# Optimization experiments

Measured on AMD Instinct MI355X. Metric: run time of the kernel, lower is better.

The kernel has to match this reference:

```python
import jax, jax.numpy as jnp
import numpy as np

B, L, C, K, NLEV, VOCAB, OUT = 32, 1024, 512, 2, 4, 128, 11


def setup_inputs() -> dict:
    key = jax.random.key(0)
    ks = jax.random.split(key, 8)
    x = jax.random.randint(ks[0], (B, L), 0, VOCAB, dtype=jnp.int32)
    mask = jax.random.randint(ks[1], (B, L), 0, 2).astype(jnp.bool_)
    emb = jax.random.uniform(ks[2], (VOCAB, C), minval=-0.5, maxval=0.5, dtype=jnp.float32)
    w1 = jax.random.normal(ks[3], (NLEV, C, C, K), dtype=jnp.float32) * 0.02
    b1 = jnp.zeros((NLEV, C), dtype=jnp.float32)
    w2 = jax.random.normal(ks[4], (NLEV, C, C, K), dtype=jnp.float32) * 0.02
    b2 = jnp.zeros((NLEV, C), dtype=jnp.float32)
    dec_w = jax.random.uniform(ks[5], (OUT, C), minval=-0.5, maxval=0.5, dtype=jnp.float32)
    dec_b = jnp.zeros((OUT,), dtype=jnp.float32)
    return dict(x=x, mask=mask, emb=emb, w1=w1, b1=b1, w2=w2, b2=b2, dec_w=dec_w, dec_b=dec_b)


def _causal_conv(h, w, b, dilation):
    # h: [B, C, L], w: [Cout, Cin, K]; left-pad (K-1)*d == conv+chomp in TCN
    pad = (w.shape[-1] - 1) * dilation
    out = jax.lax.conv_general_dilated(
        h, w, window_strides=(1,), padding=[(pad, 0)],
        rhs_dilation=(dilation,), dimension_numbers=("NCH", "OIH", "NCH"))
    return out + b[None, :, None]


def reference(x, mask, emb, w1, b1, w2, b2, dec_w, dec_b):
    h = emb[x].transpose(0, 2, 1)  # [B, C, L]
    for i in range(NLEV):  # fixed small number of TCN levels
        d = 2 ** i
        res = h
        h = jax.nn.relu(_causal_conv(h, w1[i], b1[i], d))
        h = jax.nn.relu(_causal_conv(h, w2[i], b2[i], d))
        h = jax.nn.relu(h + res)  # residual (in==out channels -> identity shortcut)
    y = jnp.einsum("bcl,oc->blo", h, dec_w) + dec_b  # [B, L, OUT]
    # mask-gather: original keeps only mask-true positions; zero others (jit-safe)
    return y * mask[..., None].astype(y.dtype)
```

## Files before the change

kernel.cpp:

```cpp
#include <hip/hip_runtime.h>
#include <stdint.h>

#define BB 32
#define LL 1024
#define CC 512
#define NN (BB * LL)
#define NLEVS 4
#define OUTD 11
#define LPAD 8
#define LROWS (LL + LPAD)

typedef __attribute__((ext_vector_type(8))) short bf16x8;
typedef __attribute__((ext_vector_type(4))) float f32x4;

static __device__ __forceinline__ unsigned short f2bf(float f) {
    union { float f; uint32_t u; } v; v.f = f;
    uint32_t u = v.u;
    uint32_t r = (u + 0x7fffu + ((u >> 16) & 1u)) >> 16;
    return (unsigned short)r;
}
static __device__ __forceinline__ float bf2f(unsigned short h) {
    union { uint32_t u; float f; } v; v.u = ((uint32_t)h) << 16;
    return v.f;
}

static __device__ __forceinline__ void llds16(const unsigned short* g, unsigned short* l) {
    __builtin_amdgcn_global_load_lds(
        (const __attribute__((address_space(1))) unsigned int*)g,
        (__attribute__((address_space(3))) unsigned int*)l, 16, 0, 0);
}

__global__ __launch_bounds__(256) void zero_pad_kernel(
    unsigned short* __restrict__ Hb0, unsigned short* __restrict__ Hb1)
{
    int t = blockIdx.x * 256 + threadIdx.x;
    unsigned short* base = (t >> 14) ? Hb1 : Hb0;
    int rem = t & 16383;
    int p = rem >> 9;
    int q = rem & 511;
    size_t off = (size_t)p * (LROWS * CC) + (size_t)q * 8;
    *(uint4*)(base + off) = (uint4){0u, 0u, 0u, 0u};
}

__global__ __launch_bounds__(256) void embed_kernel(
    const int* __restrict__ x, const float* __restrict__ emb,
    unsigned short* __restrict__ Hb0)
{
    int t = blockIdx.x * 256 + threadIdx.x;
    int n = t >> 6;
    int c8 = (t & 63) * 8;
    int idx = x[n];
    const float* src = emb + (size_t)idx * CC + c8;
    float4 v0 = *(const float4*)src;
    float4 v1 = *(const float4*)(src + 4);
    ushort4 a, b;
    a.x = f2bf(v0.x); a.y = f2bf(v0.y); a.z = f2bf(v0.z); a.w = f2bf(v0.w);
    b.x = f2bf(v1.x); b.y = f2bf(v1.y); b.z = f2bf(v1.z); b.w = f2bf(v1.w);
    int prow = (n >> 10) * LROWS + LPAD + (n & (LL - 1));
    unsigned short* dst = Hb0 + (size_t)prow * CC + c8;
    *(ushort4*)dst = a;
    *(ushort4*)(dst + 4) = b;
}

__global__ __launch_bounds__(256) void pack_w_kernel(
    const float* __restrict__ w1, const float* __restrict__ w2, unsigned short* __restrict__ WpT)
{
    int e = blockIdx.x * 256 + threadIdx.x;
    int cv = e >> 19;
    int r = e & 524287;
    int j = r >> 12;
    int co = (r >> 3) & 511;
    int h = r & 7;
    int kidx = j * 8 + h;
    int k = (kidx < 512) ? 1 : 0;
    int ci = kidx & 511;
    int lvl = cv >> 1;
    const float* w = (cv & 1) ? w2 : w1;
    float val = w[(((size_t)(lvl * 512 + co) * 512) + ci) * 2 + k];
    WpT[e] = f2bf(val);
}

__global__ __launch_bounds__(256) void pack_dw_kernel(
    const float* __restrict__ dw, unsigned short* __restrict__ dwp)
{
    int e = blockIdx.x * 256 + threadIdx.x;
    int jb = e >> 7;
    int o = (e >> 3) & 15;
    int j = e & 7;
    float val = (o < OUTD) ? dw[o * CC + jb * 8 + j] : 0.f;
    dwp[e] = f2bf(val);
}

#define SLAB (136 * 64)
template <bool HAS_RES>
__global__ __launch_bounds__(256, 4) void conv_gemm(
    const unsigned short* __restrict__ Ain, const unsigned short* __restrict__ WpT,
    const float* __restrict__ bias, const unsigned short* __restrict__ resB,
    unsigned short* __restrict__ OutB, int d)
{
    __shared__ unsigned short sA[2 * SLAB];

    const int tid = threadIdx.x;
    const int wave = tid >> 6, lane = tid & 63;

    const int bid = blockIdx.x;
    const int xcd = bid & 7;
    const int local = bid >> 3;
    const int cb = local >> 5;
    const int nb = xcd + 8 * (local & 31);
    const int co0 = cb * 128;
    const int n0 = nb * 128;

    const int rbase = (n0 >> 10) * LROWS + LPAD + (n0 & (LL - 1));
    const int wm = (wave >> 1) * 64;
    const int wn = (wave & 1) * 64;
    const int lm = lane & 15, quad = lane >> 4;

    const int r8 = lane >> 3;
    const int c8 = lane & 7;

    f32x4 acc[4][4];
#pragma unroll
    for (int i = 0; i < 4; ++i)
#pragma unroll
        for (int j = 0; j < 4; ++j) acc[i][j] = (f32x4){0.f, 0.f, 0.f, 0.f};

    for (int it = 0; it < 4; ++it) {
        const int ci0 = it * 128;

        for (int sc = wave; sc < 34; sc += 4) {
            int seg = sc >> 1, slab = sc & 1;
            int cg = slab * 8 + (c8 ^ r8);
            const unsigned short* gA =
                Ain + (size_t)(rbase - 8 + seg * 8 + r8) * CC + ci0 + cg * 8;
            llds16(gA, sA + slab * SLAB + (seg * 8) * 64);
        }
        __syncthreads();

        auto loadA = [&](int s, bf16x8* af) {
            const int t = s >> 2, ks = s & 3;
            const int shift = t ? d : 0;
            const int rowoff = 8 - shift + wm;
            const int key = (8 - shift + lm) & 7;
            const int c = ks * 4 + quad;
            const unsigned short* base = sA + (c >> 3) * SLAB + ((c & 7) ^ key) * 8;
#pragma unroll
            for (int mt = 0; mt < 4; ++mt)
                af[mt] = *(const bf16x8*)&base[(rowoff + mt * 16 + lm) * 64];
        };
        auto loadB = [&](int s, bf16x8* bf) {
            const int t = s >> 2, ks = s & 3;
            const int jb = t * 64 + it * 16 + ks * 4 + quad;
            const unsigned short* bbase = WpT + ((size_t)jb * 512 + co0 + wn + lm) * 8;
#pragma unroll
            for (int nt = 0; nt < 4; ++nt)
                bf[nt] = *(const bf16x8*)(bbase + (size_t)nt * 16 * 8);
        };

        bf16x8 afc[4], bfc[4], afn[4], bfn[4];
        loadA(0, afc);
        loadB(0, bfc);
#pragma unroll
        for (int s = 0; s < 8; ++s) {
            if (s < 7) { loadA(s + 1, afn); loadB(s + 1, bfn); }
#pragma unroll
            for (int mt = 0; mt < 4; ++mt)
#pragma unroll
                for (int nt = 0; nt < 4; ++nt)
                    acc[mt][nt] = __builtin_amdgcn_mfma_f32_16x16x32_bf16(
                        afc[mt], bfc[nt], acc[mt][nt], 0, 0, 0);
            if (s < 7) {
#pragma unroll
                for (int q2 = 0; q2 < 4; ++q2) { afc[q2] = afn[q2]; bfc[q2] = bfn[q2]; }
            }
        }
        __syncthreads();
    }

    float bv[4];
#pragma unroll
    for (int nt = 0; nt < 4; ++nt) bv[nt] = bias[co0 + wn + nt * 16 + lm];

#pragma unroll
    for (int mt = 0; mt < 4; ++mt) {
        int prow0 = rbase + wm + mt * 16 + quad * 4;
#pragma unroll
        for (int nt = 0; nt < 4; ++nt) {
            int co = co0 + wn + nt * 16 + lm;
#pragma unroll
            for (int r = 0; r < 4; ++r) {
                size_t off = (size_t)(prow0 + r) * CC + co;
                float v = acc[mt][nt][r] + bv[nt];
                v = fmaxf(v, 0.f);
                if (HAS_RES) {
                    v += bf2f(resB[off]);
                    v = fmaxf(v, 0.f);
                }
                OutB[off] = f2bf(v);
            }
        }
    }
}

__global__ __launch_bounds__(256) void decode_kernel(
    const unsigned short* __restrict__ H, const unsigned short* __restrict__ dwp,
    const float* __restrict__ db, const int* __restrict__ mask,
    float* __restrict__ out)
{
    const int wave = threadIdx.x >> 6, lane = threadIdx.x & 63;
    const int lm = lane & 15, quad = lane >> 4;
    const int n0 = blockIdx.x * 64 + wave * 16;
    const int prow = ((n0 + lm) >> 10) * LROWS + LPAD + ((n0 + lm) & (LL - 1));

    f32x4 acc = (f32x4){0.f, 0.f, 0.f, 0.f};
#pragma unroll
    for (int ks = 0; ks < 16; ++ks) {
        bf16x8 af = *(const bf16x8*)&H[(size_t)prow * CC + ks * 32 + quad * 8];
        bf16x8 bf = *(const bf16x8*)&dwp[((size_t)(ks * 4 + quad) * 16 + lm) * 8];
        acc = __builtin_amdgcn_mfma_f32_16x16x32_bf16(af, bf, acc, 0, 0, 0);
    }

    if (lm < OUTD) {
        float bo = db[lm];
#pragma unroll
        for (int r = 0; r < 4; ++r) {
            int n = n0 + quad * 4 + r;
            float v = (mask[n] != 0) ? (acc[r] + bo) : 0.f;
            out[(size_t)n * OUTD + lm] = v;
        }
    }
}

extern "C" void kernel_launch(void* const* d_in, const int* in_sizes, int n_in,
                              void* d_out, int out_size, void* d_ws, size_t ws_size,
                              hipStream_t stream)
{
    const int* x = (const int*)d_in[0];
    const int* mask = (const int*)d_in[1];
    const float* emb = (const float*)d_in[2];
    const float* w1 = (const float*)d_in[3];
    const float* b1 = (const float*)d_in[4];
    const float* w2 = (const float*)d_in[5];
    const float* b2 = (const float*)d_in[6];
    const float* dw = (const float*)d_in[7];
    const float* db = (const float*)d_in[8];
    float* out = (float*)d_out;

    char* ws = (char*)d_ws;
    const size_t HBB = (size_t)BB * LROWS * CC * 2;
    unsigned short* Hb0 = (unsigned short*)ws;
    unsigned short* Hb1 = (unsigned short*)(ws + HBB);
    unsigned short* WpT = (unsigned short*)(ws + 2 * HBB);
    unsigned short* dwp = (unsigned short*)(ws + 2 * HBB + (size_t)NLEVS * 2 * CC * 1024 * 2);

    zero_pad_kernel<<<128, 256, 0, stream>>>(Hb0, Hb1);
    embed_kernel<<<(NN * 64) / 256, 256, 0, stream>>>(x, emb, Hb0);
    pack_w_kernel<<<(NLEVS * 2 * CC * 1024) / 256, 256, 0, stream>>>(w1, w2, WpT);
    pack_dw_kernel<<<32, 256, 0, stream>>>(dw, dwp);

    const int grid = (CC / 128) * (NN / 128);
    for (int i = 0; i < NLEVS; ++i) {
        int d = 1 << i;
        const unsigned short* W1 = WpT + (size_t)(i * 2 + 0) * CC * 1024;
        const unsigned short* W2 = WpT + (size_t)(i * 2 + 1) * CC * 1024;
        conv_gemm<false><<<grid, 256, 0, stream>>>(Hb0, W1, b1 + i * CC, nullptr, Hb1, d);
        conv_gemm<true><<<grid, 256, 0, stream>>>(Hb1, W2, b2 + i * CC, Hb0, Hb0, d);
    }
    decode_kernel<<<NN / 64, 256, 0, stream>>>(Hb0, dwp, db, mask, out);
}
```

Measured before the change: 395.8 us.

## Double-buffer LDS staging in conv GEMM and merge prep kernels into one launch

The conv GEMM now stages 64-channel input chunks into two alternating LDS buffers, 8 chunks instead of 4. The load for the next chunk is issued before computing on the current one, so global-to-LDS traffic can overlap the MFMA work rather than stalling behind a barrier each iteration. Separately, the four setup kernels (weight packing, embedding, pad zeroing, decoder weight packing) are merged into one launch that dispatches on block index, removing three launch gaps. Total LDS use stays about the same, but the K loop now runs more, shorter iterations, and correctness depends on the barrier ordering around the asynchronous LDS loads.

```diff
diff --git a/kernel.cpp b/kernel.cpp
--- a/kernel.cpp
+++ b/kernel.cpp
@@ -30,75 +30,67 @@
         (__attribute__((address_space(3))) unsigned int*)l, 16, 0, 0);
 }
 
-__global__ __launch_bounds__(256) void zero_pad_kernel(
-    unsigned short* __restrict__ Hb0, unsigned short* __restrict__ Hb1)
-{
-    int t = blockIdx.x * 256 + threadIdx.x;
-    unsigned short* base = (t >> 14) ? Hb1 : Hb0;
-    int rem = t & 16383;
-    int p = rem >> 9;
-    int q = rem & 511;
-    size_t off = (size_t)p * (LROWS * CC) + (size_t)q * 8;
-    *(uint4*)(base + off) = (uint4){0u, 0u, 0u, 0u};
-}
-
-__global__ __launch_bounds__(256) void embed_kernel(
+__global__ __launch_bounds__(256) void prep_kernel(
     const int* __restrict__ x, const float* __restrict__ emb,
-    unsigned short* __restrict__ Hb0)
-{
-    int t = blockIdx.x * 256 + threadIdx.x;
-    int n = t >> 6;
-    int c8 = (t & 63) * 8;
-    int idx = x[n];
-    const float* src = emb + (size_t)idx * CC + c8;
-    float4 v0 = *(const float4*)src;
-    float4 v1 = *(const float4*)(src + 4);
-    ushort4 a, b;
-    a.x = f2bf(v0.x); a.y = f2bf(v0.y); a.z = f2bf(v0.z); a.w = f2bf(v0.w);
-    b.x = f2bf(v1.x); b.y = f2bf(v1.y); b.z = f2bf(v1.z); b.w = f2bf(v1.w);
-    int prow = (n >> 10) * LROWS + LPAD + (n & (LL - 1));
-    unsigned short* dst = Hb0 + (size_t)prow * CC + c8;
-    *(ushort4*)dst = a;
-    *(ushort4*)(dst + 4) = b;
-}
-
-__global__ __launch_bounds__(256) void pack_w_kernel(
-    const float* __restrict__ w1, const float* __restrict__ w2, unsigned short* __restrict__ WpT)
-{
-    int e = blockIdx.x * 256 + threadIdx.x;
-    int cv = e >> 19;
-    int r = e & 524287;
-    int j = r >> 12;
-    int co = (r >> 3) & 511;
-    int h = r & 7;
-    int kidx = j * 8 + h;
-    int k = (kidx < 512) ? 1 : 0;
-    int ci = kidx & 511;
-    int lvl = cv >> 1;
-    const float* w = (cv & 1) ? w2 : w1;
-    float val = w[(((size_t)(lvl * 512 + co) * 512) + ci) * 2 + k];
-    WpT[e] = f2bf(val);
-}
-
-__global__ __launch_bounds__(256) void pack_dw_kernel(
-    const float* __restrict__ dw, unsigned short* __restrict__ dwp)
-{
-    int e = blockIdx.x * 256 + threadIdx.x;
-    int jb = e >> 7;
-    int o = (e >> 3) & 15;
-    int j = e & 7;
-    float val = (o < OUTD) ? dw[o * CC + jb * 8 + j] : 0.f;
-    dwp[e] = f2bf(val);
-}
-
-#define SLAB (136 * 64)
+    const float* __restrict__ w1, const float* __restrict__ w2,
+    const float* __restrict__ dw,
+    unsigned short* __restrict__ Hb0, unsigned short* __restrict__ Hb1,
+    unsigned short* __restrict__ WpT, unsigned short* __restrict__ dwp)
+{
+    int b = blockIdx.x;
+    if (b < 16384) {
+        int e = b * 256 + threadIdx.x;
+        int cv = e >> 19;
+        int r = e & 524287;
+        int j = r >> 12;
+        int co = (r >> 3) & 511;
+        int h = r & 7;
+        int kidx = j * 8 + h;
+        int k = (kidx < 512) ? 1 : 0;
+        int ci = kidx & 511;
+        int lvl = cv >> 1;
+        const float* w = (cv & 1) ? w2 : w1;
+        WpT[e] = f2bf(w[(((size_t)(lvl * 512 + co) * 512) + ci) * 2 + k]);
+    } else if (b < 24576) {
+        int t = (b - 16384) * 256 + threadIdx.x;
+        int n = t >> 6;
+        int c8 = (t & 63) * 8;
+        int idx = x[n];
+        const float* src = emb + (size_t)idx * CC + c8;
+        float4 v0 = *(const float4*)src;
+        float4 v1 = *(const float4*)(src + 4);
+        ushort4 a, bb;
+        a.x = f2bf(v0.x); a.y = f2bf(v0.y); a.z = f2bf(v0.z); a.w = f2bf(v0.w);
+        bb.x = f2bf(v1.x); bb.y = f2bf(v1.y); bb.z = f2bf(v1.z); bb.w = f2bf(v1.w);
+        int prow = (n >> 10) * LROWS + LPAD + (n & (LL - 1));
+        unsigned short* dst = Hb0 + (size_t)prow * CC + c8;
+        *(ushort4*)dst = a;
+        *(ushort4*)(dst + 4) = bb;
+    } else if (b < 24704) {
+        int t = (b - 24576) * 256 + threadIdx.x;
+        unsigned short* base = (t >> 14) ? Hb1 : Hb0;
+        int rem = t & 16383;
+        int p = rem >> 9;
+        int q = rem & 511;
+        size_t off = (size_t)p * (LROWS * CC) + (size_t)q * 8;
+        *(uint4*)(base + off) = (uint4){0u, 0u, 0u, 0u};
+    } else {
+        int e = (b - 24704) * 256 + threadIdx.x;
+        int jb = e >> 7;
+        int o = (e >> 3) & 15;
+        int j = e & 7;
+        dwp[e] = f2bf((o < OUTD) ? dw[o * CC + jb * 8 + j] : 0.f);
+    }
+}
+
+#define BUFH (17 * 512)
 template <bool HAS_RES>
 __global__ __launch_bounds__(256, 4) void conv_gemm(
     const unsigned short* __restrict__ Ain, const unsigned short* __restrict__ WpT,
     const float* __restrict__ bias, const unsigned short* __restrict__ resB,
     unsigned short* __restrict__ OutB, int d)
 {
-    __shared__ unsigned short sA[2 * SLAB];
+    __shared__ unsigned short sA[2 * BUFH];
 
     const int tid = threadIdx.x;
     const int wave = tid >> 6, lane = tid & 63;
@@ -125,32 +117,36 @@
 #pragma unroll
         for (int j = 0; j < 4; ++j) acc[i][j] = (f32x4){0.f, 0.f, 0.f, 0.f};
 
-    for (int it = 0; it < 4; ++it) {
-        const int ci0 = it * 128;
-
-        for (int sc = wave; sc < 34; sc += 4) {
-            int seg = sc >> 1, slab = sc & 1;
-            int cg = slab * 8 + (c8 ^ r8);
-            const unsigned short* gA =
-                Ain + (size_t)(rbase - 8 + seg * 8 + r8) * CC + ci0 + cg * 8;
-            llds16(gA, sA + slab * SLAB + (seg * 8) * 64);
-        }
-        __syncthreads();
+    auto stage = [&](int it, int buf) {
+        const int ci0 = it * 64;
+        const unsigned short* gA =
+            Ain + (size_t)(rbase - 8 + r8) * CC + ci0 + (c8 ^ r8) * 8;
+        unsigned short* lbase = sA + buf * BUFH;
+        for (int seg = wave; seg < 17; seg += 4)
+            llds16(gA + (size_t)seg * 8 * CC, lbase + seg * 512);
+    };
+
+    stage(0, 0);
+    __syncthreads();
+
+    for (int it = 0; it < 8; ++it) {
+        if (it < 7) stage(it + 1, (it + 1) & 1);
+        const unsigned short* buf = sA + (it & 1) * BUFH;
+        const int jb0 = it * 8;
 
         auto loadA = [&](int s, bf16x8* af) {
-            const int t = s >> 2, ks = s & 3;
+            const int t = s >> 1, ks = s & 1;
             const int shift = t ? d : 0;
             const int rowoff = 8 - shift + wm;
             const int key = (8 - shift + lm) & 7;
-            const int c = ks * 4 + quad;
-            const unsigned short* base = sA + (c >> 3) * SLAB + ((c & 7) ^ key) * 8;
+            const int cpos = ((ks * 4 + quad) ^ key);
 #pragma unroll
             for (int mt = 0; mt < 4; ++mt)
-                af[mt] = *(const bf16x8*)&base[(rowoff + mt * 16 + lm) * 64];
+                af[mt] = *(const bf16x8*)&buf[(rowoff + mt * 16 + lm) * 64 + cpos * 8];
         };
         auto loadB = [&](int s, bf16x8* bf) {
-            const int t = s >> 2, ks = s & 3;
-            const int jb = t * 64 + it * 16 + ks * 4 + quad;
+            const int t = s >> 1, ks = s & 1;
+            const int jb = t * 64 + jb0 + ks * 4 + quad;
             const unsigned short* bbase = WpT + ((size_t)jb * 512 + co0 + wn + lm) * 8;
 #pragma unroll
             for (int nt = 0; nt < 4; ++nt)
@@ -161,15 +157,15 @@
         loadA(0, afc);
         loadB(0, bfc);
 #pragma unroll
-        for (int s = 0; s < 8; ++s) {
-            if (s < 7) { loadA(s + 1, afn); loadB(s + 1, bfn); }
+        for (int s = 0; s < 4; ++s) {
+            if (s < 3) { loadA(s + 1, afn); loadB(s + 1, bfn); }
 #pragma unroll
             for (int mt = 0; mt < 4; ++mt)
 #pragma unroll
                 for (int nt = 0; nt < 4; ++nt)
                     acc[mt][nt] = __builtin_amdgcn_mfma_f32_16x16x32_bf16(
                         afc[mt], bfc[nt], acc[mt][nt], 0, 0, 0);
-            if (s < 7) {
+            if (s < 3) {
 #pragma unroll
                 for (int q2 = 0; q2 < 4; ++q2) { afc[q2] = afn[q2]; bfc[q2] = bfn[q2]; }
             }
@@ -253,10 +249,7 @@
     unsigned short* WpT = (unsigned short*)(ws + 2 * HBB);
     unsigned short* dwp = (unsigned short*)(ws + 2 * HBB + (size_t)NLEVS * 2 * CC * 1024 * 2);
 
-    zero_pad_kernel<<<128, 256, 0, stream>>>(Hb0, Hb1);
-    embed_kernel<<<(NN * 64) / 256, 256, 0, stream>>>(x, emb, Hb0);
-    pack_w_kernel<<<(NLEVS * 2 * CC * 1024) / 256, 256, 0, stream>>>(w1, w2, WpT);
-    pack_dw_kernel<<<32, 256, 0, stream>>>(dw, dwp);
+    prep_kernel<<<24736, 256, 0, stream>>>(x, emb, w1, w2, dw, Hb0, Hb1, WpT, dwp);
 
     const int grid = (CC / 128) * (NN / 128);
     for (int i = 0; i < NLEVS; ++i) {
```

New measurement: 392.2 us. About the same (-0.9%).
